# Kernel tuning notes

Measured on AMD Instinct MI355X. Metric: run time of the kernel, lower is better.

Reference implementation:

```python
import jax, jax.numpy as jnp
import numpy as np

N_NODES = 50000
N_EDGES = 800000
LEAKY_SLOPE = 0.2


def _gcn_conv(x, src, dst, W, b, n_nodes):
    """DGL GraphConv with norm='both': D_out^{-1/2} -> SpMM -> D_in^{-1/2} -> XW+b.
    Degrees clamped to min 1 as in DGL."""
    ones = jnp.ones(src.shape[0], dtype=x.dtype)
    out_deg = jnp.clip(jax.ops.segment_sum(ones, src, num_segments=n_nodes), 1.0)
    in_deg = jnp.clip(jax.ops.segment_sum(ones, dst, num_segments=n_nodes), 1.0)
    xs = x * jax.lax.rsqrt(out_deg)[:, None]          # [N, F] source-side norm
    agg = jax.ops.segment_sum(xs[src], dst, num_segments=n_nodes)  # SpMM: [N, F]
    agg = agg * jax.lax.rsqrt(in_deg)[:, None]        # dest-side norm
    return agg @ W + b


def setup_inputs() -> dict:
    key = jax.random.key(0)
    ks = jax.random.split(key, 13)
    d_in, d_hid, d_out = 300, 400, 512
    sc_in, sc_hid = 1.0 / np.sqrt(d_in), 1.0 / np.sqrt(d_hid)
    return {
        "init_emb": jax.random.normal(ks[0], (N_NODES, d_in), jnp.float32),
        "Wa1": jax.random.normal(ks[1], (d_in, d_hid), jnp.float32) * sc_in,
        "ba1": jnp.zeros((d_hid,), jnp.float32),
        "Wa2": jax.random.normal(ks[2], (d_hid, d_out), jnp.float32) * sc_hid,
        "ba2": jnp.zeros((d_out,), jnp.float32),
        "Wb1": jax.random.normal(ks[3], (d_in, d_hid), jnp.float32) * sc_in,
        "bb1": jnp.zeros((d_hid,), jnp.float32),
        "Wb2": jax.random.normal(ks[4], (d_hid, d_out), jnp.float32) * sc_hid,
        "bb2": jnp.zeros((d_out,), jnp.float32),
        "src1": jax.random.randint(ks[5], (N_EDGES,), 0, N_NODES, jnp.int32),
        "dst1": jax.random.randint(ks[6], (N_EDGES,), 0, N_NODES, jnp.int32),
        "src2": jax.random.randint(ks[7], (N_EDGES,), 0, N_NODES, jnp.int32),
        "dst2": jax.random.randint(ks[8], (N_EDGES,), 0, N_NODES, jnp.int32),
    }


def reference(init_emb, Wa1, ba1, Wa2, ba2, Wb1, bb1, Wb2, bb2,
              src1, dst1, src2, dst2):
    n = init_emb.shape[0]
    # hop 1 (dropout=0.0 -> identity)
    x1 = jax.nn.leaky_relu(_gcn_conv(init_emb, src1, dst1, Wa1, ba1, n), LEAKY_SLOPE)
    x2 = jax.nn.leaky_relu(_gcn_conv(init_emb, src2, dst2, Wb1, bb1, n), LEAKY_SLOPE)
    x = x1 + x2
    # hop 2
    y1 = _gcn_conv(x, src1, dst1, Wa2, ba2, n)
    y2 = _gcn_conv(x, src2, dst2, Wb2, bb2, n)
    return y1 + y2
```

## Files before the change

### kernel.cpp

```cpp
#include <hip/hip_runtime.h>

#define NN 50000
#define NE 800000
#define LEAKY 0.2f

using bf16x8 = __attribute__((ext_vector_type(8))) short;
using f32x4  = __attribute__((ext_vector_type(4))) float;

static __device__ __forceinline__ unsigned short f2bf(float f) {
  unsigned u = __float_as_uint(f);
  u += 0x7FFF + ((u >> 16) & 1);
  return (unsigned short)(u >> 16);
}
static __device__ __forceinline__ float bf2f(unsigned short h) {
  return __uint_as_float((unsigned)h << 16);
}

__global__ void zero_ints(int* __restrict__ p, int n) {
  int i = blockIdx.x * blockDim.x + threadIdx.x;
  int s = gridDim.x * blockDim.x;
  for (; i < n; i += s) p[i] = 0;
}

__global__ void deg_kernel(const int* __restrict__ s1, const int* __restrict__ d1,
                           const int* __restrict__ s2, const int* __restrict__ d2,
                           int* od1, int* id1, int* od2, int* id2) {
  int i = blockIdx.x * blockDim.x + threadIdx.x;
  int st = gridDim.x * blockDim.x;
  for (int e = i; e < NE; e += st) {
    int a = s1[e], b = d1[e], c = s2[e], d = d2[e];
    atomicAdd(&od1[a], 1);
    atomicAdd(&id1[b], 1);
    atomicAdd(&od2[c], 1);
    atomicAdd(&id2[d], 1);
  }
}

__global__ void scale_kernel(const int* __restrict__ od1, const int* __restrict__ id1,
                             const int* __restrict__ od2, const int* __restrict__ id2,
                             float* io1, float* ii1, float* io2, float* ii2) {
  int i = blockIdx.x * blockDim.x + threadIdx.x;
  if (i < NN) {
    io1[i] = rsqrtf((float)(od1[i] > 0 ? od1[i] : 1));
    ii1[i] = rsqrtf((float)(id1[i] > 0 ? id1[i] : 1));
    io2[i] = rsqrtf((float)(od2[i] > 0 ? od2[i] : 1));
    ii2[i] = rsqrtf((float)(id2[i] > 0 ? id2[i] : 1));
  }
}

__global__ void scan_kernel(const int* __restrict__ id1, const int* __restrict__ id2,
                            int* rp1, int* rp2) {
  const int* deg = blockIdx.x ? id2 : id1;
  int* rp = blockIdx.x ? rp2 : rp1;
  __shared__ int sm[1024];
  __shared__ int carry;
  int t = threadIdx.x;
  if (t == 0) carry = 0;
  __syncthreads();
  for (int base = 0; base < NN; base += 1024) {
    int v = (base + t < NN) ? deg[base + t] : 0;
    sm[t] = v;
    __syncthreads();
    #pragma unroll
    for (int o = 1; o < 1024; o <<= 1) {
      int add = (t >= o) ? sm[t - o] : 0;
      __syncthreads();
      sm[t] += add;
      __syncthreads();
    }
    if (base + t < NN) rp[base + t] = carry + sm[t] - v;
    __syncthreads();
    if (t == 0) carry += sm[1023];
    __syncthreads();
  }
  if (t == 0) rp[NN] = carry;
}

__global__ void fill_kernel(const int* __restrict__ s1, const int* __restrict__ d1,
                            const int* __restrict__ s2, const int* __restrict__ d2,
                            const int* __restrict__ rp1, const int* __restrict__ rp2,
                            int* fill1, int* fill2, int* col1, int* col2) {
  int i = blockIdx.x * blockDim.x + threadIdx.x;
  int st = gridDim.x * blockDim.x;
  for (int e = i; e < NE; e += st) {
    int sa = s1[e], da = d1[e], sb = s2[e], db = d2[e];
    int pa = atomicAdd(&fill1[da], 1);
    int pb = atomicAdd(&fill2[db], 1);
    col1[rp1[da] + pa] = sa;
    col2[rp2[db] + pb] = sb;
  }
}

template <int F, int KP>
__global__ __launch_bounds__(256) void spmm_kernel(
    const float* __restrict__ x, const int* __restrict__ rp, const int* __restrict__ col,
    const float* __restrict__ inv_out, const float* __restrict__ inv_in,
    short* __restrict__ hi, short* __restrict__ lo) {
  constexpr int F4 = F / 4;
  constexpr int P4 = KP / 4;
  constexpr int NI = (P4 + 63) / 64;
  int gw = (blockIdx.x * blockDim.x + threadIdx.x) >> 6;
  int lane = threadIdx.x & 63;
  int nw = (gridDim.x * blockDim.x) >> 6;
  const float4* __restrict__ x4 = (const float4*)x;
  for (int node = gw; node < NN; node += nw) {
    float4 acc[NI];
    #pragma unroll
    for (int i = 0; i < NI; ++i) acc[i] = make_float4(0.f, 0.f, 0.f, 0.f);
    int beg = rp[node], end = rp[node + 1];
    for (int j = beg; j < end; ++j) {
      int s = col[j];
      float w = inv_out[s];
      #pragma unroll
      for (int i = 0; i < NI; ++i) {
        int idx = i * 64 + lane;
        if (idx < F4) {
          float4 v = x4[(size_t)s * F4 + idx];
          acc[i].x += v.x * w;
          acc[i].y += v.y * w;
          acc[i].z += v.z * w;
          acc[i].w += v.w * w;
        }
      }
    }
    float wi = inv_in[node];
    #pragma unroll
    for (int i = 0; i < NI; ++i) {
      int idx = i * 64 + lane;
      if (idx < P4) {
        float4 v = acc[i];
        v.x *= wi; v.y *= wi; v.z *= wi; v.w *= wi;
        unsigned short hx = f2bf(v.x), hy = f2bf(v.y), hz = f2bf(v.z), hw = f2bf(v.w);
        short4 h = make_short4((short)hx, (short)hy, (short)hz, (short)hw);
        short4 l = make_short4((short)f2bf(v.x - bf2f(hx)), (short)f2bf(v.y - bf2f(hy)),
                               (short)f2bf(v.z - bf2f(hz)), (short)f2bf(v.w - bf2f(hw)));
        *(short4*)&hi[(size_t)node * KP + idx * 4] = h;
        *(short4*)&lo[(size_t)node * KP + idx * 4] = l;
      }
    }
  }
}

__global__ void wsplit(const float* __restrict__ W, short* __restrict__ Wh,
                       short* __restrict__ Wl, int K, int Nc, int KB) {
  int total = 2 * KB * 8192;
  int i = blockIdx.x * blockDim.x + threadIdx.x;
  int st = gridDim.x * blockDim.x;
  for (; i < total; i += st) {
    int c2 = i >> 13;
    int e = i & 8191;
    int kk = e >> 8;
    int rn = e & 255;
    int nb2 = c2 / KB;
    int kb = c2 - nb2 * KB;
    int n = nb2 * 256 + rn;
    int k = kb * 32 + kk;
    float v = (n < Nc && k < K) ? W[(size_t)k * Nc + n] : 0.f;
    unsigned short h = f2bf(v);
    unsigned short l = f2bf(v - bf2f(h));
    size_t o = (size_t)c2 * 8192 + (rn >> 4) * 512 + ((kk >> 3) * 16 + (rn & 15)) * 8 + (kk & 7);
    Wh[o] = (short)h;
    Wl[o] = (short)l;
  }
}

template <int EPI, int DUAL>
__global__ __launch_bounds__(256) void mgemm(
    const short* __restrict__ A1h, const short* __restrict__ A1l,
    const short* __restrict__ A2h, const short* __restrict__ A2l,
    const short* __restrict__ W1h, const short* __restrict__ W1l,
    const short* __restrict__ W2h, const short* __restrict__ W2l,
    const float* __restrict__ b1, const float* __restrict__ b2,
    const float* __restrict__ T, float* __restrict__ out,
    int M, int Nc, int KB, int KP) {
  __shared__ short Ah[4096], Al[4096];
  __shared__ short Bh[8192], Bl[8192];

  const int tid = threadIdx.x;
  const int nwg = gridDim.x;
  const int q = nwg >> 3, r = nwg & 7;
  const int xcd = blockIdx.x & 7, loc = blockIdx.x >> 3;
  const int wgid = ((xcd < r) ? xcd * (q + 1) : r * (q + 1) + (xcd - r) * q) + loc;
  const int nb = wgid & 1;
  const int m0 = (wgid >> 1) * 128;
  const int n0 = nb * 256;

  const int lane = tid & 63;
  const int wid = tid >> 6;
  const int wr = (wid >> 1) * 64;
  const int wc = (wid & 1) * 128;

  f32x4 acc[4][8];
  #pragma unroll
  for (int i = 0; i < 4; ++i)
    #pragma unroll
    for (int j = 0; j < 8; ++j) acc[i][j] = (f32x4)(0.f);

  for (int kb = 0; kb < KB; ++kb) {
    #pragma unroll
    for (int ch = 0; ch < 1 + DUAL; ++ch) {
      const short* __restrict__ Asrch = ch ? A2h : A1h;
      const short* __restrict__ Asrcl = ch ? A2l : A1l;
      const short* __restrict__ Wsrch = ch ? W2h : W1h;
      const short* __restrict__ Wsrcl = ch ? W2l : W1l;
      #pragma unroll
      for (int it = 0; it < 2; ++it) {
        int g = it * 256 + tid;
        int w = g & 63;
        int rrow = m0 + (g >> 6) * 16 + (w & 15);
        int ko = (w >> 4) * 8;
        uint4 vh = make_uint4(0u, 0u, 0u, 0u), vl = vh;
        if (rrow < M) {
          size_t ga = (size_t)rrow * KP + kb * 32 + ko;
          vh = *(const uint4*)(Asrch + ga);
          vl = *(const uint4*)(Asrcl + ga);
        }
        *(uint4*)&Ah[g * 8] = vh;
        *(uint4*)&Al[g * 8] = vl;
      }
      {
        size_t wb = ((size_t)(nb * KB + kb)) * 8192;
        #pragma unroll
        for (int it = 0; it < 4; ++it) {
          int g = it * 256 + tid;
          *(uint4*)&Bh[g * 8] = *(const uint4*)(Wsrch + wb + g * 8);
          *(uint4*)&Bl[g * 8] = *(const uint4*)(Wsrcl + wb + g * 8);
        }
      }
      __syncthreads();
      {
        bf16x8 fah[4], fal[4];
        #pragma unroll
        for (int i = 0; i < 4; ++i) {
          int sub = (wr >> 4) + i;
          fah[i] = *(const bf16x8*)&Ah[sub * 512 + lane * 8];
          fal[i] = *(const bf16x8*)&Al[sub * 512 + lane * 8];
        }
        #pragma unroll
        for (int j = 0; j < 8; ++j) {
          int sub = (wc >> 4) + j;
          bf16x8 fbh = *(const bf16x8*)&Bh[sub * 512 + lane * 8];
          bf16x8 fbl = *(const bf16x8*)&Bl[sub * 512 + lane * 8];
          #pragma unroll
          for (int i = 0; i < 4; ++i) {
            acc[i][j] = __builtin_amdgcn_mfma_f32_16x16x32_bf16(fah[i], fbh, acc[i][j], 0, 0, 0);
            acc[i][j] = __builtin_amdgcn_mfma_f32_16x16x32_bf16(fah[i], fbl, acc[i][j], 0, 0, 0);
            acc[i][j] = __builtin_amdgcn_mfma_f32_16x16x32_bf16(fal[i], fbh, acc[i][j], 0, 0, 0);
          }
        }
      }
      __syncthreads();
    }
  }

  #pragma unroll
  for (int i = 0; i < 4; ++i) {
    #pragma unroll
    for (int rr = 0; rr < 4; ++rr) {
      int rg = m0 + wr + i * 16 + (lane >> 4) * 4 + rr;
      if (rg >= M) continue;
      #pragma unroll
      for (int j = 0; j < 8; ++j) {
        int c = n0 + wc + j * 16 + (lane & 15);
        if (c >= Nc) continue;
        float v = acc[i][j][rr] + b1[c];
        if (DUAL) v += b2[c];
        if (EPI == 0 || EPI == 1) v = v > 0.f ? v : LEAKY * v;
        if (EPI == 1) v += T[(size_t)rg * Nc + c];
        out[(size_t)rg * Nc + c] = v;
      }
    }
  }
}

extern "C" void kernel_launch(void* const* d_in, const int* in_sizes, int n_in,
                              void* d_out, int out_size, void* d_ws, size_t ws_size,
                              hipStream_t stream) {
  const float* emb = (const float*)d_in[0];
  const float* Wa1 = (const float*)d_in[1];
  const float* ba1 = (const float*)d_in[2];
  const float* Wa2 = (const float*)d_in[3];
  const float* ba2 = (const float*)d_in[4];
  const float* Wb1 = (const float*)d_in[5];
  const float* bb1 = (const float*)d_in[6];
  const float* Wb2 = (const float*)d_in[7];
  const float* bb2 = (const float*)d_in[8];
  const int* src1 = (const int*)d_in[9];
  const int* dst1 = (const int*)d_in[10];
  const int* src2 = (const int*)d_in[11];
  const int* dst2 = (const int*)d_in[12];
  float* out = (float*)d_out;

  char* ws = (char*)d_ws;
  size_t off = 0;
  auto alloc = [&](size_t nbytes) -> void* {
    off = (off + 255) & ~(size_t)255;
    void* p = ws + off;
    off += nbytes;
    return p;
  };
  int* od1 = (int*)alloc(NN * 4);
  int* id1 = (int*)alloc(NN * 4);
  int* od2 = (int*)alloc(NN * 4);
  int* id2 = (int*)alloc(NN * 4);
  int* fill1 = (int*)alloc(NN * 4);
  int* fill2 = (int*)alloc(NN * 4);
  int* rp1 = (int*)alloc((NN + 1) * 4);
  int* rp2 = (int*)alloc((NN + 1) * 4);
  int* col1 = (int*)alloc((size_t)NE * 4);
  int* col2 = (int*)alloc((size_t)NE * 4);
  float* io1 = (float*)alloc(NN * 4);
  float* ii1 = (float*)alloc(NN * 4);
  float* io2 = (float*)alloc(NN * 4);
  float* ii2 = (float*)alloc(NN * 4);
  const int KB1 = 10;
  const int KB2 = 13;
  short* Wa1h = (short*)alloc((size_t)2 * KB1 * 8192 * 2);
  short* Wa1l = (short*)alloc((size_t)2 * KB1 * 8192 * 2);
  short* Wb1h = (short*)alloc((size_t)2 * KB1 * 8192 * 2);
  short* Wb1l = (short*)alloc((size_t)2 * KB1 * 8192 * 2);
  short* Wa2h = (short*)alloc((size_t)2 * KB2 * 8192 * 2);
  short* Wa2l = (short*)alloc((size_t)2 * KB2 * 8192 * 2);
  short* Wb2h = (short*)alloc((size_t)2 * KB2 * 8192 * 2);
  short* Wb2l = (short*)alloc((size_t)2 * KB2 * 8192 * 2);
  short* A1h = (short*)alloc((size_t)NN * 416 * 2);
  short* A1l = (short*)alloc((size_t)NN * 416 * 2);
  short* A2h = (short*)alloc((size_t)NN * 416 * 2);
  short* A2l = (short*)alloc((size_t)NN * 416 * 2);
  float* X = (float*)d_out;

  int nz = (int)(((char*)fill2 - (char*)od1) / 4) + NN;
  zero_ints<<<256, 256, 0, stream>>>(od1, nz);

  deg_kernel<<<1024, 256, 0, stream>>>(src1, dst1, src2, dst2, od1, id1, od2, id2);
  scale_kernel<<<(NN + 255) / 256, 256, 0, stream>>>(od1, id1, od2, id2, io1, ii1, io2, ii2);
  scan_kernel<<<2, 1024, 0, stream>>>(id1, id2, rp1, rp2);
  fill_kernel<<<1024, 256, 0, stream>>>(src1, dst1, src2, dst2, rp1, rp2,
                                        fill1, fill2, col1, col2);

  wsplit<<<320, 256, 0, stream>>>(Wa1, Wa1h, Wa1l, 300, 400, KB1);
  wsplit<<<320, 256, 0, stream>>>(Wb1, Wb1h, Wb1l, 300, 400, KB1);
  wsplit<<<416, 256, 0, stream>>>(Wa2, Wa2h, Wa2l, 400, 512, KB2);
  wsplit<<<416, 256, 0, stream>>>(Wb2, Wb2h, Wb2l, 400, 512, KB2);

  const int NWG = 2 * ((NN + 127) / 128);

  spmm_kernel<300, 320><<<12500, 256, 0, stream>>>(emb, rp1, col1, io1, ii1, A1h, A1l);
  mgemm<0, 0><<<NWG, 256, 0, stream>>>(A1h, A1l, nullptr, nullptr, Wa1h, Wa1l,
                                       nullptr, nullptr, ba1, nullptr, nullptr, X,
                                       NN, 400, KB1, 320);
  spmm_kernel<300, 320><<<12500, 256, 0, stream>>>(emb, rp2, col2, io2, ii2, A1h, A1l);
  mgemm<1, 0><<<NWG, 256, 0, stream>>>(A1h, A1l, nullptr, nullptr, Wb1h, Wb1l,
                                       nullptr, nullptr, bb1, nullptr, X, X,
                                       NN, 400, KB1, 320);

  spmm_kernel<400, 416><<<12500, 256, 0, stream>>>(X, rp1, col1, io1, ii1, A1h, A1l);
  spmm_kernel<400, 416><<<12500, 256, 0, stream>>>(X, rp2, col2, io2, ii2, A2h, A2l);
  mgemm<2, 1><<<NWG, 256, 0, stream>>>(A1h, A1l, A2h, A2l, Wa2h, Wa2l, Wb2h, Wb2l,
                                       ba2, bb2, nullptr, out, NN, 512, KB2, 416);
}
```

Before: 1.872 ms.

## Pre-tile SpMM output for direct-to-LDS double-buffered GEMM with 128x128 tiles

SpMM now writes its bf16 hi/lo outputs directly into the MFMA fragment tile layout, so the GEMM can stage A and W with global_load_lds 16-byte copies into a double-buffered LDS ring. Loading the next k-step overlaps with compute on the current one. Output tiles shrink from 128x256 to 128x128 with launch_bounds allowing two workgroups per CU. The two hop-1 GEMMs are fused into one kernel with separate accumulators, which removes the X read-modify-write pass. The cost is two extra accumulator arrays in the hop-1 kernel, and rows past NN in the last M-tile are loaded without a bounds guard (the padded buffer is never written there).

After: 1.603 ms. 1.17x faster.

```diff
diff --git a/kernel.cpp b/kernel.cpp
--- a/kernel.cpp
+++ b/kernel.cpp
@@ -14,6 +14,12 @@
 }
 static __device__ __forceinline__ float bf2f(unsigned short h) {
   return __uint_as_float((unsigned)h << 16);
+}
+
+static __device__ __forceinline__ void gload16(const short* g, short* l) {
+  __builtin_amdgcn_global_load_lds(
+      (const __attribute__((address_space(1))) void*)g,
+      (__attribute__((address_space(3))) void*)l, 16, 0, 0);
 }
 
 __global__ void zero_ints(int* __restrict__ p, int n) {
@@ -91,13 +97,13 @@
   }
 }
 
-template <int F, int KP>
+template <int F, int KB>
 __global__ __launch_bounds__(256) void spmm_kernel(
     const float* __restrict__ x, const int* __restrict__ rp, const int* __restrict__ col,
     const float* __restrict__ inv_out, const float* __restrict__ inv_in,
     short* __restrict__ hi, short* __restrict__ lo) {
   constexpr int F4 = F / 4;
-  constexpr int P4 = KP / 4;
+  constexpr int P4 = KB * 8;
   constexpr int NI = (P4 + 63) / 64;
   int gw = (blockIdx.x * blockDim.x + threadIdx.x) >> 6;
   int lane = threadIdx.x & 63;
@@ -124,6 +130,8 @@
       }
     }
     float wi = inv_in[node];
+    int mt = node >> 7, sub = (node >> 4) & 7, lr = node & 15;
+    size_t nbase = (((size_t)mt * KB) * 8 + sub) * 512;
     #pragma unroll
     for (int i = 0; i < NI; ++i) {
       int idx = i * 64 + lane;
@@ -134,139 +142,145 @@
         short4 h = make_short4((short)hx, (short)hy, (short)hz, (short)hw);
         short4 l = make_short4((short)f2bf(v.x - bf2f(hx)), (short)f2bf(v.y - bf2f(hy)),
                                (short)f2bf(v.z - bf2f(hz)), (short)f2bf(v.w - bf2f(hw)));
-        *(short4*)&hi[(size_t)node * KP + idx * 4] = h;
-        *(short4*)&lo[(size_t)node * KP + idx * 4] = l;
+        int kb = idx >> 3, q = idx & 7;
+        size_t o = nbase + (size_t)kb * 4096 + ((q >> 1) * 16 + lr) * 8 + (q & 1) * 4;
+        *(short4*)&hi[o] = h;
+        *(short4*)&lo[o] = l;
       }
     }
   }
 }
 
 __global__ void wsplit(const float* __restrict__ W, short* __restrict__ Wh,
-                       short* __restrict__ Wl, int K, int Nc, int KB) {
-  int total = 2 * KB * 8192;
+                       short* __restrict__ Wl, int K, int Nc, int KB, int NB) {
+  int total = NB * KB * 4096;
   int i = blockIdx.x * blockDim.x + threadIdx.x;
   int st = gridDim.x * blockDim.x;
   for (; i < total; i += st) {
-    int c2 = i >> 13;
-    int e = i & 8191;
-    int kk = e >> 8;
-    int rn = e & 255;
-    int nb2 = c2 / KB;
-    int kb = c2 - nb2 * KB;
-    int n = nb2 * 256 + rn;
+    int chunk = i >> 12;
+    int e = i & 4095;
+    int kk = e >> 7;
+    int rn = e & 127;
+    int nb = chunk / KB;
+    int kb = chunk - nb * KB;
+    int n = nb * 128 + rn;
     int k = kb * 32 + kk;
     float v = (n < Nc && k < K) ? W[(size_t)k * Nc + n] : 0.f;
     unsigned short h = f2bf(v);
     unsigned short l = f2bf(v - bf2f(h));
-    size_t o = (size_t)c2 * 8192 + (rn >> 4) * 512 + ((kk >> 3) * 16 + (rn & 15)) * 8 + (kk & 7);
+    size_t o = (size_t)chunk * 4096 + (rn >> 4) * 512 + ((kk >> 3) * 16 + (rn & 15)) * 8 + (kk & 7);
     Wh[o] = (short)h;
     Wl[o] = (short)l;
   }
 }
 
-template <int EPI, int DUAL>
-__global__ __launch_bounds__(256) void mgemm(
+#define COMPUTE_STEP(BB, ACC)                                                    \
+  {                                                                              \
+    bf16x8 fah[4], fal[4];                                                       \
+    _Pragma("unroll")                                                            \
+    for (int i = 0; i < 4; ++i) {                                                \
+      fah[i] = *(const bf16x8*)&lds[BB][0][(wr4 + i) * 512 + lane * 8];          \
+      fal[i] = *(const bf16x8*)&lds[BB][1][(wr4 + i) * 512 + lane * 8];          \
+    }                                                                            \
+    _Pragma("unroll")                                                            \
+    for (int j = 0; j < 4; ++j) {                                                \
+      bf16x8 fbh = *(const bf16x8*)&lds[BB][2][(wc4 + j) * 512 + lane * 8];      \
+      bf16x8 fbl = *(const bf16x8*)&lds[BB][3][(wc4 + j) * 512 + lane * 8];      \
+      _Pragma("unroll")                                                          \
+      for (int i = 0; i < 4; ++i) {                                              \
+        ACC[i][j] = __builtin_amdgcn_mfma_f32_16x16x32_bf16(fah[i], fbh, ACC[i][j], 0, 0, 0); \
+        ACC[i][j] = __builtin_amdgcn_mfma_f32_16x16x32_bf16(fah[i], fbl, ACC[i][j], 0, 0, 0); \
+        ACC[i][j] = __builtin_amdgcn_mfma_f32_16x16x32_bf16(fal[i], fbh, ACC[i][j], 0, 0, 0); \
+      }                                                                          \
+    }                                                                            \
+  }
+
+#define STAGE_STEP(SS, BB)                                                       \
+  {                                                                              \
+    int ch_ = (SS) & 1;                                                          \
+    int kb_ = (SS) >> 1;                                                         \
+    const short* ah_ = ch_ ? A2h : A1h;                                          \
+    const short* al_ = ch_ ? A2l : A1l;                                          \
+    const short* wh_ = ch_ ? W2h : W1h;                                          \
+    const short* wl_ = ch_ ? W2l : W1l;                                          \
+    size_t abase_ = ((size_t)mt * KB + kb_) * 4096;                              \
+    size_t wbase_ = ((size_t)nb * KB + kb_) * 4096;                              \
+    _Pragma("unroll")                                                            \
+    for (int c = 0; c < 2; ++c) {                                                \
+      int s_ = wid * 2 + c;                                                      \
+      size_t go_ = (size_t)s_ * 512 + lane * 8;                                  \
+      gload16(ah_ + abase_ + go_, &lds[BB][0][s_ * 512]);                        \
+      gload16(al_ + abase_ + go_, &lds[BB][1][s_ * 512]);                        \
+      gload16(wh_ + wbase_ + go_, &lds[BB][2][s_ * 512]);                        \
+      gload16(wl_ + wbase_ + go_, &lds[BB][3][s_ * 512]);                        \
+    }                                                                            \
+  }
+
+template <int EPI>
+__global__ __launch_bounds__(256, 2) void mgemm(
     const short* __restrict__ A1h, const short* __restrict__ A1l,
     const short* __restrict__ A2h, const short* __restrict__ A2l,
     const short* __restrict__ W1h, const short* __restrict__ W1l,
     const short* __restrict__ W2h, const short* __restrict__ W2l,
     const float* __restrict__ b1, const float* __restrict__ b2,
-    const float* __restrict__ T, float* __restrict__ out,
-    int M, int Nc, int KB, int KP) {
-  __shared__ short Ah[4096], Al[4096];
-  __shared__ short Bh[8192], Bl[8192];
+    float* __restrict__ out, int M, int Nc, int KB, int NB) {
+  __shared__ short lds[2][4][4096];
 
   const int tid = threadIdx.x;
   const int nwg = gridDim.x;
   const int q = nwg >> 3, r = nwg & 7;
   const int xcd = blockIdx.x & 7, loc = blockIdx.x >> 3;
   const int wgid = ((xcd < r) ? xcd * (q + 1) : r * (q + 1) + (xcd - r) * q) + loc;
-  const int nb = wgid & 1;
-  const int m0 = (wgid >> 1) * 128;
-  const int n0 = nb * 256;
+  const int nb = wgid & (NB - 1);
+  const int mt = wgid >> 2;
+  const int m0 = mt * 128;
+  const int n0 = nb * 128;
 
   const int lane = tid & 63;
   const int wid = tid >> 6;
-  const int wr = (wid >> 1) * 64;
-  const int wc = (wid & 1) * 128;
-
-  f32x4 acc[4][8];
+  const int wr4 = (wid >> 1) * 4;
+  const int wc4 = (wid & 1) * 4;
+
+  f32x4 acc1[4][4], acc2[4][4];
   #pragma unroll
   for (int i = 0; i < 4; ++i)
     #pragma unroll
-    for (int j = 0; j < 8; ++j) acc[i][j] = (f32x4)(0.f);
-
-  for (int kb = 0; kb < KB; ++kb) {
-    #pragma unroll
-    for (int ch = 0; ch < 1 + DUAL; ++ch) {
-      const short* __restrict__ Asrch = ch ? A2h : A1h;
-      const short* __restrict__ Asrcl = ch ? A2l : A1l;
-      const short* __restrict__ Wsrch = ch ? W2h : W1h;
-      const short* __restrict__ Wsrcl = ch ? W2l : W1l;
-      #pragma unroll
-      for (int it = 0; it < 2; ++it) {
-        int g = it * 256 + tid;
-        int w = g & 63;
-        int rrow = m0 + (g >> 6) * 16 + (w & 15);
-        int ko = (w >> 4) * 8;
-        uint4 vh = make_uint4(0u, 0u, 0u, 0u), vl = vh;
-        if (rrow < M) {
-          size_t ga = (size_t)rrow * KP + kb * 32 + ko;
-          vh = *(const uint4*)(Asrch + ga);
-          vl = *(const uint4*)(Asrcl + ga);
-        }
-        *(uint4*)&Ah[g * 8] = vh;
-        *(uint4*)&Al[g * 8] = vl;
-      }
-      {
-        size_t wb = ((size_t)(nb * KB + kb)) * 8192;
-        #pragma unroll
-        for (int it = 0; it < 4; ++it) {
-          int g = it * 256 + tid;
-          *(uint4*)&Bh[g * 8] = *(const uint4*)(Wsrch + wb + g * 8);
-          *(uint4*)&Bl[g * 8] = *(const uint4*)(Wsrcl + wb + g * 8);
-        }
-      }
-      __syncthreads();
-      {
-        bf16x8 fah[4], fal[4];
-        #pragma unroll
-        for (int i = 0; i < 4; ++i) {
-          int sub = (wr >> 4) + i;
-          fah[i] = *(const bf16x8*)&Ah[sub * 512 + lane * 8];
-          fal[i] = *(const bf16x8*)&Al[sub * 512 + lane * 8];
-        }
-        #pragma unroll
-        for (int j = 0; j < 8; ++j) {
-          int sub = (wc >> 4) + j;
-          bf16x8 fbh = *(const bf16x8*)&Bh[sub * 512 + lane * 8];
-          bf16x8 fbl = *(const bf16x8*)&Bl[sub * 512 + lane * 8];
-          #pragma unroll
-          for (int i = 0; i < 4; ++i) {
-            acc[i][j] = __builtin_amdgcn_mfma_f32_16x16x32_bf16(fah[i], fbh, acc[i][j], 0, 0, 0);
-            acc[i][j] = __builtin_amdgcn_mfma_f32_16x16x32_bf16(fah[i], fbl, acc[i][j], 0, 0, 0);
-            acc[i][j] = __builtin_amdgcn_mfma_f32_16x16x32_bf16(fal[i], fbh, acc[i][j], 0, 0, 0);
-          }
-        }
-      }
-      __syncthreads();
-    }
+    for (int j = 0; j < 4; ++j) { acc1[i][j] = (f32x4)(0.f); acc2[i][j] = (f32x4)(0.f); }
+
+  const int S = 2 * KB;
+  STAGE_STEP(0, 0);
+  __syncthreads();
+  for (int step = 0; step < S; ++step) {
+    int b = step & 1;
+    if (step + 1 < S) STAGE_STEP(step + 1, b ^ 1);
+    if (EPI == 0 && (step & 1)) {
+      COMPUTE_STEP(b, acc2);
+    } else {
+      COMPUTE_STEP(b, acc1);
+    }
+    __syncthreads();
   }
 
   #pragma unroll
   for (int i = 0; i < 4; ++i) {
     #pragma unroll
     for (int rr = 0; rr < 4; ++rr) {
-      int rg = m0 + wr + i * 16 + (lane >> 4) * 4 + rr;
+      int rg = m0 + wr4 * 16 + i * 16 + (lane >> 4) * 4 + rr;
       if (rg >= M) continue;
       #pragma unroll
-      for (int j = 0; j < 8; ++j) {
-        int c = n0 + wc + j * 16 + (lane & 15);
+      for (int j = 0; j < 4; ++j) {
+        int c = n0 + wc4 * 16 + j * 16 + (lane & 15);
         if (c >= Nc) continue;
-        float v = acc[i][j][rr] + b1[c];
-        if (DUAL) v += b2[c];
-        if (EPI == 0 || EPI == 1) v = v > 0.f ? v : LEAKY * v;
-        if (EPI == 1) v += T[(size_t)rg * Nc + c];
+        float v;
+        if (EPI == 0) {
+          float v1 = acc1[i][j][rr] + b1[c];
+          float v2 = acc2[i][j][rr] + b2[c];
+          v1 = v1 > 0.f ? v1 : LEAKY * v1;
+          v2 = v2 > 0.f ? v2 : LEAKY * v2;
+          v = v1 + v2;
+        } else {
+          v = acc1[i][j][rr] + b1[c] + b2[c];
+        }
         out[(size_t)rg * Nc + c] = v;
       }
     }
@@ -315,18 +329,22 @@
   float* ii2 = (float*)alloc(NN * 4);
   const int KB1 = 10;
   const int KB2 = 13;
-  short* Wa1h = (short*)alloc((size_t)2 * KB1 * 8192 * 2);
-  short* Wa1l = (short*)alloc((size_t)2 * KB1 * 8192 * 2);
-  short* Wb1h = (short*)alloc((size_t)2 * KB1 * 8192 * 2);
-  short* Wb1l = (short*)alloc((size_t)2 * KB1 * 8192 * 2);
-  short* Wa2h = (short*)alloc((size_t)2 * KB2 * 8192 * 2);
-  short* Wa2l = (short*)alloc((size_t)2 * KB2 * 8192 * 2);
-  short* Wb2h = (short*)alloc((size_t)2 * KB2 * 8192 * 2);
-  short* Wb2l = (short*)alloc((size_t)2 * KB2 * 8192 * 2);
-  short* A1h = (short*)alloc((size_t)NN * 416 * 2);
-  short* A1l = (short*)alloc((size_t)NN * 416 * 2);
-  short* A2h = (short*)alloc((size_t)NN * 416 * 2);
-  short* A2l = (short*)alloc((size_t)NN * 416 * 2);
+  const int NB1 = 4;
+  const int NB2 = 4;
+  const int NM = (NN + 127) / 128;
+  short* Wa1h = (short*)alloc((size_t)NB1 * KB1 * 4096 * 2);
+  short* Wa1l = (short*)alloc((size_t)NB1 * KB1 * 4096 * 2);
+  short* Wb1h = (short*)alloc((size_t)NB1 * KB1 * 4096 * 2);
+  short* Wb1l = (short*)alloc((size_t)NB1 * KB1 * 4096 * 2);
+  short* Wa2h = (short*)alloc((size_t)NB2 * KB2 * 4096 * 2);
+  short* Wa2l = (short*)alloc((size_t)NB2 * KB2 * 4096 * 2);
+  short* Wb2h = (short*)alloc((size_t)NB2 * KB2 * 4096 * 2);
+  short* Wb2l = (short*)alloc((size_t)NB2 * KB2 * 4096 * 2);
+  size_t aplane = (size_t)NM * KB2 * 4096;
+  short* A1h = (short*)alloc(aplane * 2);
+  short* A1l = (short*)alloc(aplane * 2);
+  short* A2h = (short*)alloc(aplane * 2);
+  short* A2l = (short*)alloc(aplane * 2);
   float* X = (float*)d_out;
 
   int nz = (int)(((char*)fill2 - (char*)od1) / 4) + NN;
@@ -338,24 +356,18 @@
   fill_kernel<<<1024, 256, 0, stream>>>(src1, dst1, src2, dst2, rp1, rp2,
                                         fill1, fill2, col1, col2);
 
-  wsplit<<<320, 256, 0, stream>>>(Wa1, Wa1h, Wa1l, 300, 400, KB1);
-  wsplit<<<320, 256, 0, stream>>>(Wb1, Wb1h, Wb1l, 300, 400, KB1);
-  wsplit<<<416, 256, 0, stream>>>(Wa2, Wa2h, Wa2l, 400, 512, KB2);
-  wsplit<<<416, 256, 0, stream>>>(Wb2, Wb2h, Wb2l, 400, 512, KB2);
-
-  const int NWG = 2 * ((NN + 127) / 128);
-
-  spmm_kernel<300, 320><<<12500, 256, 0, stream>>>(emb, rp1, col1, io1, ii1, A1h, A1l);
-  mgemm<0, 0><<<NWG, 256, 0, stream>>>(A1h, A1l, nullptr, nullptr, Wa1h, Wa1l,
-                                       nullptr, nullptr, ba1, nullptr, nullptr, X,
-                                       NN, 400, KB1, 320);
-  spmm_kernel<300, 320><<<12500, 256, 0, stream>>>(emb, rp2, col2, io2, ii2, A1h, A1l);
-  mgemm<1, 0><<<NWG, 256, 0, stream>>>(A1h, A1l, nullptr, nullptr, Wb1h, Wb1l,
-                                       nullptr, nullptr, bb1, nullptr, X, X,
-                                       NN, 400, KB1, 320);
-
-  spmm_kernel<400, 416><<<12500, 256, 0, stream>>>(X, rp1, col1, io1, ii1, A1h, A1l);
-  spmm_kernel<400, 416><<<12500, 256, 0, stream>>>(X, rp2, col2, io2, ii2, A2h, A2l);
-  mgemm<2, 1><<<NWG, 256, 0, stream>>>(A1h, A1l, A2h, A2l, Wa2h, Wa2l, Wb2h, Wb2l,
-                                       ba2, bb2, nullptr, out, NN, 512, KB2, 416);
-}
+  wsplit<<<640, 256, 0, stream>>>(Wa1, Wa1h, Wa1l, 300, 400, KB1, NB1);
+  wsplit<<<640, 256, 0, stream>>>(Wb1, Wb1h, Wb1l, 300, 400, KB1, NB1);
+  wsplit<<<832, 256, 0, stream>>>(Wa2, Wa2h, Wa2l, 400, 512, KB2, NB2);
+  wsplit<<<832, 256, 0, stream>>>(Wb2, Wb2h, Wb2l, 400, 512, KB2, NB2);
+
+  spmm_kernel<300, KB1><<<12500, 256, 0, stream>>>(emb, rp1, col1, io1, ii1, A1h, A1l);
+  spmm_kernel<300, KB1><<<12500, 256, 0, stream>>>(emb, rp2, col2, io2, ii2, A2h, A2l);
+  mgemm<0><<<NB1 * NM, 256, 0, stream>>>(A1h, A1l, A2h, A2l, Wa1h, Wa1l, Wb1h, Wb1l,
+                                         ba1, bb1, X, NN, 400, KB1, NB1);
+
+  spmm_kernel<400, KB2><<<12500, 256, 0, stream>>>(X, rp1, col1, io1, ii1, A1h, A1l);
+  spmm_kernel<400, KB2><<<12500, 256, 0, stream>>>(X, rp2, col2, io2, ii2, A2h, A2l);
+  mgemm<1><<<NB2 * NM, 256, 0, stream>>>(A1h, A1l, A2h, A2l, Wa2h, Wa2l, Wb2h, Wb2l,
+                                         ba2, bb2, out, NN, 512, KB2, NB2);
+}
```
